# Kernel optimization log

Measured on AMD Instinct MI355X. Metric: run time of the kernel, lower is better.

## Reference

```python
import jax, jax.numpy as jnp
import numpy as np
from jax.scipy.special import logsumexp

N, C = 8192, 4096
LOSS_WEIGHT = 1.0


def setup_inputs() -> dict:
    key = jax.random.key(0)
    k1, k2 = jax.random.split(key)
    cls_score = jax.random.normal(k1, (N, C), dtype=jnp.float32)
    label = jax.random.randint(k2, (N, C), 0, 2, dtype=jnp.int64)
    return {"cls_score": cls_score, "label": label}


def reference(cls_score, label):
    # pos/neg masks exactly as in the torch module
    pos = label >= 1
    neg = label == 0
    ninf = -jnp.inf
    # Torch builds an [N, C*C] tensor of (neg_k - pos_j) padded with a 0 column
    # and takes logsumexp over it. Algebraically:
    #   loss_i = logaddexp(0, logsumexp_k(pred[neg]) + logsumexp_j(-pred[pos]))
    lse_neg = logsumexp(jnp.where(neg, cls_score, ninf), axis=1)      # [N]
    lse_mpos = logsumexp(jnp.where(pos, -cls_score, ninf), axis=1)    # [N]
    loss = jnp.logaddexp(jnp.float32(0.0), lse_neg + lse_mpos)        # [N]
    # reduction='mean', loss_weight applied in forward
    return LOSS_WEIGHT * jnp.mean(loss)
```

## Files before the change

### kernel.cpp

```cpp
#include <hip/hip_runtime.h>
#include <hip/hip_bf16.h>
#include <float.h>

#define NROWS 8192
#define NCOLS 4096


__global__ __launch_bounds__(256) void row_loss_kernel(
        const float* __restrict__ score,
        const int* __restrict__ label,
        float* __restrict__ row_loss) {
    const int row = blockIdx.x;
    const int t = threadIdx.x;

    const float4* __restrict__ srow = reinterpret_cast<const float4*>(score + (size_t)row * NCOLS);
    const int4*   __restrict__ lrow = reinterpret_cast<const int4*>(label + (size_t)row * NCOLS);

    float4 f0 = srow[t + 0 * 256];
    float4 f1 = srow[t + 1 * 256];
    float4 f2 = srow[t + 2 * 256];
    float4 f3 = srow[t + 3 * 256];
    int4 l0 = lrow[t + 0 * 256];
    int4 l1 = lrow[t + 1 * 256];
    int4 l2 = lrow[t + 2 * 256];
    int4 l3 = lrow[t + 3 * 256];

    float x[16] = {f0.x, f0.y, f0.z, f0.w, f1.x, f1.y, f1.z, f1.w,
                   f2.x, f2.y, f2.z, f2.w, f3.x, f3.y, f3.z, f3.w};
    int   l[16] = {l0.x, l0.y, l0.z, l0.w, l1.x, l1.y, l1.z, l1.w,
                   l2.x, l2.y, l2.z, l2.w, l3.x, l3.y, l3.z, l3.w};

    float s_n = 0.0f, s_p = 0.0f;
#pragma unroll
    for (int k = 0; k < 16; ++k) {
        bool neg = (l[k] == 0);
        float e = __expf(neg ? x[k] : -x[k]);
        s_n += neg ? e : 0.0f;
        s_p += neg ? 0.0f : e;
    }

#pragma unroll
    for (int off = 32; off > 0; off >>= 1) {
        s_n += __shfl_down(s_n, off, 64);
        s_p += __shfl_down(s_p, off, 64);
    }

    __shared__ float ls[4][2];
    const int wave = t >> 6;
    if ((t & 63) == 0) {
        ls[wave][0] = s_n;
        ls[wave][1] = s_p;
    }
    __syncthreads();

    if (t == 0) {
        float S_n = ls[0][0] + ls[1][0] + ls[2][0] + ls[3][0];
        float S_p = ls[0][1] + ls[1][1] + ls[2][1] + ls[3][1];
        float loss;
        if (S_n <= 0.0f || S_p <= 0.0f) {
            loss = 0.0f;
        } else {
            float z = logf(S_n) + logf(S_p);
            loss = fmaxf(z, 0.0f) + log1pf(__expf(-fabsf(z)));
        }
        row_loss[row] = loss;
    }
}

__global__ __launch_bounds__(256) void mean_kernel(
        const float* __restrict__ row_loss,
        float* __restrict__ out) {
    const int t = threadIdx.x;
    const float4* rl = reinterpret_cast<const float4*>(row_loss);
    float s = 0.0f;
#pragma unroll
    for (int j = 0; j < NROWS / 4 / 256; ++j) {
        float4 v = rl[t + j * 256];
        s += (v.x + v.y) + (v.z + v.w);
    }
#pragma unroll
    for (int off = 32; off > 0; off >>= 1) s += __shfl_down(s, off, 64);
    __shared__ float ls[4];
    if ((t & 63) == 0) ls[t >> 6] = s;
    __syncthreads();
    if (t == 0) {
        float total = ls[0] + ls[1] + ls[2] + ls[3];
        out[0] = total * (1.0f / (float)NROWS);
    }
}

extern "C" void kernel_launch(void* const* d_in, const int* in_sizes, int n_in,
                              void* d_out, int out_size, void* d_ws, size_t ws_size,
                              hipStream_t stream) {
    const float* score = (const float*)d_in[0];
    const int*   label = (const int*)d_in[1];
    float* row_loss = (float*)d_ws;
    float* out = (float*)d_out;

    row_loss_kernel<<<NROWS, 256, 0, stream>>>(score, label, row_loss);
    mean_kernel<<<1, 256, 0, stream>>>(row_loss, out);
}
```

Measured before the change: 274.5 us.

## Process one row per wavefront with double-buffered loads

Each 64-lane wavefront now owns a full row, so each block handles four rows and the grid shrinks by four. This removes the shared-memory exchange and block barrier in the row reduction. Loads are issued in groups of four float4/int4 pairs, with the next group fetched before the current one is reduced, to keep more memory requests in flight. Each lane now streams 64 elements instead of 16 and holds more registers.

```diff
diff --git a/kernel.cpp b/kernel.cpp
--- a/kernel.cpp
+++ b/kernel.cpp
@@ -6,38 +6,54 @@
 #define NCOLS 4096
 
 
+__device__ __forceinline__ void accum_group(const float4* f, const int4* l,
+                                            float& s_n, float& s_p) {
+#pragma unroll
+    for (int j = 0; j < 4; ++j) {
+        float x[4] = {f[j].x, f[j].y, f[j].z, f[j].w};
+        int   m[4] = {l[j].x, l[j].y, l[j].z, l[j].w};
+#pragma unroll
+        for (int k = 0; k < 4; ++k) {
+            bool neg = (m[k] == 0);
+            float e = __expf(neg ? x[k] : -x[k]);
+            s_n += neg ? e : 0.0f;
+            s_p += neg ? 0.0f : e;
+        }
+    }
+}
+
 __global__ __launch_bounds__(256) void row_loss_kernel(
         const float* __restrict__ score,
         const int* __restrict__ label,
         float* __restrict__ row_loss) {
-    const int row = blockIdx.x;
-    const int t = threadIdx.x;
+    const int wave = threadIdx.x >> 6;
+    const int lane = threadIdx.x & 63;
+    const int row  = blockIdx.x * 4 + wave;
 
     const float4* __restrict__ srow = reinterpret_cast<const float4*>(score + (size_t)row * NCOLS);
     const int4*   __restrict__ lrow = reinterpret_cast<const int4*>(label + (size_t)row * NCOLS);
 
-    float4 f0 = srow[t + 0 * 256];
-    float4 f1 = srow[t + 1 * 256];
-    float4 f2 = srow[t + 2 * 256];
-    float4 f3 = srow[t + 3 * 256];
-    int4 l0 = lrow[t + 0 * 256];
-    int4 l1 = lrow[t + 1 * 256];
-    int4 l2 = lrow[t + 2 * 256];
-    int4 l3 = lrow[t + 3 * 256];
+    float4 fa[4], fb[4];
+    int4   la[4], lb[4];
 
-    float x[16] = {f0.x, f0.y, f0.z, f0.w, f1.x, f1.y, f1.z, f1.w,
-                   f2.x, f2.y, f2.z, f2.w, f3.x, f3.y, f3.z, f3.w};
-    int   l[16] = {l0.x, l0.y, l0.z, l0.w, l1.x, l1.y, l1.z, l1.w,
-                   l2.x, l2.y, l2.z, l2.w, l3.x, l3.y, l3.z, l3.w};
+#pragma unroll
+    for (int j = 0; j < 4; ++j) {
+        fa[j] = srow[lane + j * 64];
+        la[j] = lrow[lane + j * 64];
+    }
 
     float s_n = 0.0f, s_p = 0.0f;
+
 #pragma unroll
-    for (int k = 0; k < 16; ++k) {
-        bool neg = (l[k] == 0);
-        float e = __expf(neg ? x[k] : -x[k]);
-        s_n += neg ? e : 0.0f;
-        s_p += neg ? 0.0f : e;
-    }
+    for (int j = 0; j < 4; ++j) { fb[j] = srow[256 + lane + j * 64]; lb[j] = lrow[256 + lane + j * 64]; }
+    accum_group(fa, la, s_n, s_p);
+#pragma unroll
+    for (int j = 0; j < 4; ++j) { fa[j] = srow[512 + lane + j * 64]; la[j] = lrow[512 + lane + j * 64]; }
+    accum_group(fb, lb, s_n, s_p);
+#pragma unroll
+    for (int j = 0; j < 4; ++j) { fb[j] = srow[768 + lane + j * 64]; lb[j] = lrow[768 + lane + j * 64]; }
+    accum_group(fa, la, s_n, s_p);
+    accum_group(fb, lb, s_n, s_p);
 
 #pragma unroll
     for (int off = 32; off > 0; off >>= 1) {
@@ -45,22 +61,12 @@
         s_p += __shfl_down(s_p, off, 64);
     }
 
-    __shared__ float ls[4][2];
-    const int wave = t >> 6;
-    if ((t & 63) == 0) {
-        ls[wave][0] = s_n;
-        ls[wave][1] = s_p;
-    }
-    __syncthreads();
-
-    if (t == 0) {
-        float S_n = ls[0][0] + ls[1][0] + ls[2][0] + ls[3][0];
-        float S_p = ls[0][1] + ls[1][1] + ls[2][1] + ls[3][1];
+    if (lane == 0) {
         float loss;
-        if (S_n <= 0.0f || S_p <= 0.0f) {
+        if (s_n <= 0.0f || s_p <= 0.0f) {
             loss = 0.0f;
         } else {
-            float z = logf(S_n) + logf(S_p);
+            float z = logf(s_n) + logf(s_p);
             loss = fmaxf(z, 0.0f) + log1pf(__expf(-fabsf(z)));
         }
         row_loss[row] = loss;
@@ -97,6 +103,6 @@
     float* row_loss = (float*)d_ws;
     float* out = (float*)d_out;
 
-    row_loss_kernel<<<NROWS, 256, 0, stream>>>(score, label, row_loss);
+    row_loss_kernel<<<NROWS / 4, 256, 0, stream>>>(score, label, row_loss);
     mean_kernel<<<1, 256, 0, stream>>>(row_loss, out);
 }
```

Result: no change. 276.8 us (+0.8%).
